# Kernel optimization log

Measured on AMD Instinct MI355X. Metric: run time of the kernel, lower is better.

Reference implementation:

```python
import jax, jax.numpy as jnp
import numpy as np

B, L, N, D = 16, 4096, 1024, 256
EPS = 1e-5
NEG = -1e9


def setup_inputs() -> dict:
    key = jax.random.key(0)
    k1, k2, k3 = jax.random.split(key, 3)
    exp_f = jax.random.normal(k1, (B, L, D), dtype=jnp.float32)
    Q = jax.random.normal(k2, (B, N, D), dtype=jnp.float32)
    attn_mask = jax.random.randint(k3, (B, L, N), 0, 2).astype(jnp.bool_)
    gamma = jnp.ones((D,), dtype=jnp.float32)
    beta = jnp.zeros((D,), dtype=jnp.float32)
    return {"exp_f": exp_f, "Q": Q, "attn_mask": attn_mask, "gamma": gamma, "beta": beta}


def layer_norm(x, gamma, beta):
    mu = jnp.mean(x, axis=-1, keepdims=True)
    var = jnp.mean(jnp.square(x - mu), axis=-1, keepdims=True)
    return (x - mu) * jax.lax.rsqrt(var + EPS) * gamma + beta


def reference(exp_f, Q, attn_mask, gamma, beta):
    d_k = Q.shape[-1]
    scale = 1.0 / np.sqrt(d_k).astype(np.float32)
    # scores: [B, L, N] = exp_f @ Q^T / sqrt(d)
    scores = jnp.einsum('bld,bnd->bln', exp_f, Q) * scale
    scores = jnp.where(attn_mask, jnp.float32(NEG), scores)
    # transpose to [B, N, L], softmax over L (text positions)
    attn = jax.nn.softmax(scores.transpose(0, 2, 1), axis=-1)
    # context: [B, N, D]
    context = jnp.einsum('bnl,bld->bnd', attn, exp_f)
    return layer_norm(Q + context, gamma, beta)
```

## Files before the change

kernel.cpp:

```cpp
#include <hip/hip_runtime.h>
#include <hip/hip_bf16.h>
#include <math.h>

typedef short bf16x8 __attribute__((ext_vector_type(8)));
typedef float f32x4 __attribute__((ext_vector_type(4)));
typedef unsigned int u32;
typedef unsigned short u16;

#define B_ 16
#define L_ 4096
#define N_ 1024
#define D_ 256
#define EPS_ 1e-5f
#define NEG_ -1.0e9f
#define LOG2E_ 1.4426950408889634f
#define THR_ 8.0f

#define LBLK 32
#define ESTR2 264
#define TSTR2 40
#define PSTR2 40

__device__ __forceinline__ u32 pk2(float x, float y) {
  __hip_bfloat16 hx = __float2bfloat16(x), hy = __float2bfloat16(y);
  return (u32)reinterpret_cast<unsigned short&>(hx) |
         ((u32)reinterpret_cast<unsigned short&>(hy) << 16);
}
__device__ __forceinline__ float bf2f(u16 u) {
  return __uint_as_float(((u32)u) << 16);
}

__global__ __launch_bounds__(256)
void prep_kernel(const float* __restrict__ ef, __hip_bfloat16* __restrict__ et,
                 __hip_bfloat16* __restrict__ ebf, int write_ebf) {
  __shared__ float T[64][65];
  const int tid = threadIdx.x;
  const int bid = blockIdx.x;
  const int b  = bid >> 8;
  const int lt = (bid >> 2) & 63;
  const int dt = bid & 3;
  {
    const int r = tid & 63, s = tid >> 6;
    const float* src = ef + ((size_t)b * L_ + lt * 64 + r) * D_ + dt * 64 + s * 16;
    float v[16];
    #pragma unroll
    for (int k = 0; k < 4; ++k) {
      float4 f = *reinterpret_cast<const float4*>(src + 4 * k);
      v[4*k] = f.x; v[4*k+1] = f.y; v[4*k+2] = f.z; v[4*k+3] = f.w;
    }
    #pragma unroll
    for (int m = 0; m < 16; ++m) T[r][s * 16 + m] = v[m];
    if (write_ebf) {
      u32 w[8];
      #pragma unroll
      for (int p = 0; p < 8; ++p) w[p] = pk2(v[2*p], v[2*p+1]);
      __hip_bfloat16* dst = ebf + ((size_t)b * L_ + lt * 64 + r) * D_ + dt * 64 + s * 16;
      *reinterpret_cast<uint4*>(dst)     = *reinterpret_cast<uint4*>(&w[0]);
      *reinterpret_cast<uint4*>(dst + 8) = *reinterpret_cast<uint4*>(&w[4]);
    }
  }
  __syncthreads();
  {
    const int dcol = tid & 63, s2 = tid >> 6;
    float v[16];
    #pragma unroll
    for (int m = 0; m < 16; ++m) v[m] = T[s2 * 16 + m][dcol];
    u32 w[8];
    #pragma unroll
    for (int p = 0; p < 8; ++p) w[p] = pk2(v[2*p], v[2*p+1]);
    __hip_bfloat16* dst = et + ((size_t)b * D_ + dt * 64 + dcol) * L_ + lt * 64 + s2 * 16;
    *reinterpret_cast<uint4*>(dst)     = *reinterpret_cast<uint4*>(&w[0]);
    *reinterpret_cast<uint4*>(dst + 8) = *reinterpret_cast<uint4*>(&w[4]);
  }
}

__global__ __launch_bounds__(256, 2)
void attn_part2(const float* __restrict__ ef, const float* __restrict__ q,
                const int* __restrict__ msk, const __hip_bfloat16* __restrict__ et,
                const __hip_bfloat16* __restrict__ ebf, int use_ebf, int slog,
                __hip_bfloat16* __restrict__ opart,
                float* __restrict__ mpart, float* __restrict__ lpart) {
  extern __shared__ char smem[];
  __hip_bfloat16* EL  = (__hip_bfloat16*)smem;
  __hip_bfloat16* TL  = EL + LBLK * ESTR2;
  __hip_bfloat16* PLb = TL + 256 * TSTR2;

  const int tid  = threadIdx.x;
  const int wid  = tid >> 6;
  const int lane = tid & 63;
  const int g    = lane >> 4;
  const int c    = lane & 15;

  const int S   = 1 << slog;
  const int nb  = 128 << slog;
  const int raw = blockIdx.x;
  const int cpx = nb >> 3;
  const int bs  = (raw & 7) * cpx + (raw >> 3);
  const int nt   = bs & 7;
  const int rest = bs >> 3;
  const int s    = rest & (S - 1);
  const int b    = rest >> slog;

  const int lsplit = L_ >> slog;
  const int lbase  = s * lsplit;
  const int n0w    = nt * 128 + wid * 32;

  bf16x8 qf[2][8];
  #pragma unroll
  for (int h = 0; h < 2; ++h) {
    const float* qrow = q + ((size_t)b * N_ + n0w + 16*h + c) * D_;
    #pragma unroll
    for (int dk = 0; dk < 8; ++dk) {
      float4 a  = *reinterpret_cast<const float4*>(qrow + 32 * dk + 8 * g);
      float4 b2 = *reinterpret_cast<const float4*>(qrow + 32 * dk + 8 * g + 4);
      u32 w[4] = {pk2(a.x, a.y), pk2(a.z, a.w), pk2(b2.x, b2.y), pk2(b2.z, b2.w)};
      qf[h][dk] = *reinterpret_cast<bf16x8*>(w);
    }
  }

  f32x4 oacc[2][16];
  float m_run[2], l_run[2];
  #pragma unroll
  for (int h = 0; h < 2; ++h) {
    m_run[h] = -INFINITY; l_run[h] = 0.f;
    #pragma unroll
    for (int j = 0; j < 16; ++j) oacc[h][j] = (f32x4){0.f, 0.f, 0.f, 0.f};
  }

  __hip_bfloat16* PLw = PLb + wid * (2 * 16 * PSTR2);
  const float scale = 0.0625f;
  const int ntiles = lsplit / LBLK;

  for (int t = 0; t < ntiles; ++t) {
    const int l0 = lbase + t * LBLK;

    __syncthreads();

    #pragma unroll
    for (int p = 0; p < 4; ++p) {
      const int unit = tid + 256 * p;
      const int row = unit >> 5, iu = unit & 31;
      if (use_ebf) {
        *reinterpret_cast<uint4*>(EL + row * ESTR2 + iu * 8) =
            *reinterpret_cast<const uint4*>(ebf + ((size_t)b * L_ + l0 + row) * D_ + iu * 8);
      } else {
        const float* src = ef + ((size_t)b * L_ + l0 + row) * D_ + iu * 8;
        float4 a  = *reinterpret_cast<const float4*>(src);
        float4 b2 = *reinterpret_cast<const float4*>(src + 4);
        u32 w[4] = {pk2(a.x, a.y), pk2(a.z, a.w), pk2(b2.x, b2.y), pk2(b2.z, b2.w)};
        *reinterpret_cast<uint4*>(EL + row * ESTR2 + iu * 8) =
            *reinterpret_cast<uint4*>(w);
      }
    }
    #pragma unroll
    for (int p = 0; p < 4; ++p) {
      const int unit = tid + 256 * p;
      const int dr = unit >> 2, iu = unit & 3;
      *reinterpret_cast<uint4*>(TL + dr * TSTR2 + iu * 8) =
          *reinterpret_cast<const uint4*>(et + ((size_t)b * D_ + dr) * L_ + l0 + iu * 8);
    }

    int mv[16];
    #pragma unroll
    for (int h = 0; h < 2; ++h)
      #pragma unroll
      for (int tt = 0; tt < 2; ++tt)
        #pragma unroll
        for (int r = 0; r < 4; ++r)
          mv[8*h + 4*tt + r] =
              msk[((size_t)b * L_ + l0 + 16*tt + 4*g + r) * N_ + n0w + 16*h + c];

    __syncthreads();

    float sv[2][8];
    #pragma unroll
    for (int tt = 0; tt < 2; ++tt) {
      f32x4 s0 = (f32x4){0.f, 0.f, 0.f, 0.f};
      f32x4 s1 = (f32x4){0.f, 0.f, 0.f, 0.f};
      #pragma unroll
      for (int dk = 0; dk < 8; ++dk) {
        bf16x8 af = *reinterpret_cast<const bf16x8*>(EL + (16*tt + c) * ESTR2 + 32*dk + 8*g);
        s0 = __builtin_amdgcn_mfma_f32_16x16x32_bf16(af, qf[0][dk], s0, 0, 0, 0);
        s1 = __builtin_amdgcn_mfma_f32_16x16x32_bf16(af, qf[1][dk], s1, 0, 0, 0);
      }
      #pragma unroll
      for (int r = 0; r < 4; ++r) {
        float v0 = s0[r] * scale;
        float v1 = s1[r] * scale;
        if (mv[4*tt + r])     v0 = NEG_;
        if (mv[8 + 4*tt + r]) v1 = NEG_;
        sv[0][4*tt + r] = v0;
        sv[1][4*tt + r] = v1;
      }
    }

    #pragma unroll
    for (int h = 0; h < 2; ++h) {
      float tm = sv[h][0];
      #pragma unroll
      for (int i = 1; i < 8; ++i) tm = fmaxf(tm, sv[h][i]);
      tm = fmaxf(tm, __shfl_xor(tm, 16));
      tm = fmaxf(tm, __shfl_xor(tm, 32));
      if (!__all(tm - m_run[h] <= THR_)) {
        const float mn = fmaxf(m_run[h], tm);
        const float alpha = __builtin_amdgcn_exp2f((m_run[h] - mn) * LOG2E_);
        l_run[h] *= alpha;
        float ar[4];
        #pragma unroll
        for (int r = 0; r < 4; ++r) ar[r] = __shfl(alpha, 4*g + r, 64);
        #pragma unroll
        for (int j = 0; j < 16; ++j)
          #pragma unroll
          for (int r = 0; r < 4; ++r) oacc[h][j][r] *= ar[r];
        m_run[h] = mn;
      }
      float ts = 0.f;
      #pragma unroll
      for (int i = 0; i < 8; ++i) {
        sv[h][i] = __builtin_amdgcn_exp2f((sv[h][i] - m_run[h]) * LOG2E_);
        ts += sv[h][i];
      }
      ts += __shfl_xor(ts, 16);
      ts += __shfl_xor(ts, 32);
      l_run[h] += ts;
      #pragma unroll
      for (int tt = 0; tt < 2; ++tt) {
        uint2 w;
        w.x = pk2(sv[h][4*tt+0], sv[h][4*tt+1]);
        w.y = pk2(sv[h][4*tt+2], sv[h][4*tt+3]);
        *reinterpret_cast<uint2*>(PLw + h * 16 * PSTR2 + c * PSTR2 + 16*tt + 4*g) = w;
      }
    }

    bf16x8 pa0 = *reinterpret_cast<const bf16x8*>(PLw + c * PSTR2 + 8*g);
    bf16x8 pa1 = *reinterpret_cast<const bf16x8*>(PLw + 16 * PSTR2 + c * PSTR2 + 8*g);
    #pragma unroll
    for (int j = 0; j < 16; ++j) {
      bf16x8 bfr = *reinterpret_cast<const bf16x8*>(TL + (16*j + c) * TSTR2 + 8*g);
      oacc[0][j] = __builtin_amdgcn_mfma_f32_16x16x32_bf16(pa0, bfr, oacc[0][j], 0, 0, 0);
      oacc[1][j] = __builtin_amdgcn_mfma_f32_16x16x32_bf16(pa1, bfr, oacc[1][j], 0, 0, 0);
    }
  }

  const size_t slot = (size_t)rest * 8 + nt;
  __hip_bfloat16* ob = opart + slot * (128 * 256);
  #pragma unroll
  for (int h = 0; h < 2; ++h) {
    float invl[4];
    #pragma unroll
    for (int r = 0; r < 4; ++r) invl[r] = 1.f / __shfl(l_run[h], 4*g + r, 64);
    #pragma unroll
    for (int r = 0; r < 4; ++r) {
      const int row = wid * 32 + 16*h + 4*g + r;
      #pragma unroll
      for (int j = 0; j < 16; ++j)
        ob[(size_t)row * 256 + 16*j + c] = __float2bfloat16(oacc[h][j][r] * invl[r]);
    }
  }
  if (g == 0) {
    #pragma unroll
    for (int h = 0; h < 2; ++h) {
      mpart[slot * 128 + wid * 32 + 16*h + c] = m_run[h];
      lpart[slot * 128 + wid * 32 + 16*h + c] = l_run[h];
    }
  }
}

__global__ __launch_bounds__(256)
void combine_ln2(const float* __restrict__ q, const float* __restrict__ gamma,
                 const float* __restrict__ beta,
                 const __hip_bfloat16* __restrict__ opart,
                 const float* __restrict__ mpart, const float* __restrict__ lpart,
                 int S, float* __restrict__ out) {
  const int tid = threadIdx.x, wid = tid >> 6, lane = tid & 63;
  const int row = blockIdx.x * 4 + wid;
  const int b = row >> 10, n = row & 1023;
  const int ntile = n >> 7, nl = n & 127;

  float M = -INFINITY;
  for (int s = 0; s < S; ++s) {
    const size_t slot = (size_t)(b * S + s) * 8 + ntile;
    M = fmaxf(M, mpart[slot * 128 + nl]);
  }
  float W = 0.f;
  float4 o = make_float4(0.f, 0.f, 0.f, 0.f);
  for (int s = 0; s < S; ++s) {
    const size_t slot = (size_t)(b * S + s) * 8 + ntile;
    const float w = __builtin_amdgcn_exp2f((mpart[slot * 128 + nl] - M) * LOG2E_) *
                    lpart[slot * 128 + nl];
    W += w;
    ushort4 ov = *reinterpret_cast<const ushort4*>(
        opart + (slot * 128 + nl) * 256 + lane * 4);
    o.x += w * bf2f(ov.x); o.y += w * bf2f(ov.y);
    o.z += w * bf2f(ov.z); o.w += w * bf2f(ov.w);
  }
  const float invW = 1.f / W;
  float4 qv = *reinterpret_cast<const float4*>(q + ((size_t)b * N_ + n) * D_ + lane * 4);
  float4 x;
  x.x = qv.x + o.x * invW; x.y = qv.y + o.y * invW;
  x.z = qv.z + o.z * invW; x.w = qv.w + o.w * invW;

  float sum = x.x + x.y + x.z + x.w;
  sum += __shfl_xor(sum, 1);  sum += __shfl_xor(sum, 2);
  sum += __shfl_xor(sum, 4);  sum += __shfl_xor(sum, 8);
  sum += __shfl_xor(sum, 16); sum += __shfl_xor(sum, 32);
  const float mu = sum * (1.f / 256.f);
  float dx, v2 = 0.f;
  dx = x.x - mu; v2 += dx * dx; dx = x.y - mu; v2 += dx * dx;
  dx = x.z - mu; v2 += dx * dx; dx = x.w - mu; v2 += dx * dx;
  v2 += __shfl_xor(v2, 1);  v2 += __shfl_xor(v2, 2);
  v2 += __shfl_xor(v2, 4);  v2 += __shfl_xor(v2, 8);
  v2 += __shfl_xor(v2, 16); v2 += __shfl_xor(v2, 32);
  const float rs = rsqrtf(v2 * (1.f / 256.f) + EPS_);
  float4 gv = *reinterpret_cast<const float4*>(gamma + lane * 4);
  float4 bv = *reinterpret_cast<const float4*>(beta + lane * 4);
  float4 y;
  y.x = (x.x - mu) * rs * gv.x + bv.x;
  y.y = (x.y - mu) * rs * gv.y + bv.y;
  y.z = (x.z - mu) * rs * gv.z + bv.z;
  y.w = (x.w - mu) * rs * gv.w + bv.w;
  *reinterpret_cast<float4*>(out + ((size_t)b * N_ + n) * D_ + lane * 4) = y;
}

#define QSTRIDE (D_ + 4)
#define PSTRIDF (64 + 4)
__global__ __launch_bounds__(256)
void tgq_fallback(const float* __restrict__ ef, const float* __restrict__ q,
                  const int* __restrict__ msk, const float* __restrict__ gamma,
                  const float* __restrict__ beta, float* __restrict__ out) {
  extern __shared__ float fsm[];
  float* QL = fsm;
  float* EL = QL + 64 * QSTRIDE;
  float* PL = EL + 64 * QSTRIDE;
  const int tid = threadIdx.x, tx = tid & 15, ty = tid >> 4;
  const int b = blockIdx.x >> 4, n0 = (blockIdx.x & 15) * 64;
  {
    const float* qsrc = q + ((size_t)b * N_ + n0) * D_;
    for (int idx = tid; idx < 64 * 64; idx += 256) {
      int row = idx >> 6, c4 = idx & 63;
      *reinterpret_cast<float4*>(&QL[row * QSTRIDE + c4 * 4]) =
          *reinterpret_cast<const float4*>(qsrc + (size_t)row * D_ + c4 * 4);
    }
  }
  float4 O4[4][4]; float m_run[4], l_run[4];
  #pragma unroll
  for (int i = 0; i < 4; ++i) {
    m_run[i] = -INFINITY; l_run[i] = 0.f;
    #pragma unroll
    for (int k = 0; k < 4; ++k) O4[i][k] = make_float4(0.f, 0.f, 0.f, 0.f);
  }
  const float* efb = ef + (size_t)b * L_ * D_;
  const int* mb = msk + (size_t)b * L_ * N_;
  for (int t = 0; t < L_ / 64; ++t) {
    const int l0 = t * 64;
    __syncthreads();
    for (int idx = tid; idx < 64 * 64; idx += 256) {
      int row = idx >> 6, c4 = idx & 63;
      *reinterpret_cast<float4*>(&EL[row * QSTRIDE + c4 * 4]) =
          *reinterpret_cast<const float4*>(efb + (size_t)(l0 + row) * D_ + c4 * 4);
    }
    int4 mvv[4];
    #pragma unroll
    for (int j = 0; j < 4; ++j)
      mvv[j] = *reinterpret_cast<const int4*>(mb + (size_t)(l0 + tx + 16*j) * N_ + n0 + 4*ty);
    __syncthreads();
    float s0[4][4];
    #pragma unroll
    for (int i = 0; i < 4; ++i)
      #pragma unroll
      for (int j = 0; j < 4; ++j) s0[i][j] = 0.f;
    #pragma unroll 4
    for (int dq = 0; dq < 64; ++dq) {
      float4 qv[4], ev[4];
      #pragma unroll
      for (int i = 0; i < 4; ++i)
        qv[i] = *reinterpret_cast<const float4*>(&QL[(4*ty+i) * QSTRIDE + dq*4]);
      #pragma unroll
      for (int j = 0; j < 4; ++j)
        ev[j] = *reinterpret_cast<const float4*>(&EL[(tx+16*j) * QSTRIDE + dq*4]);
      #pragma unroll
      for (int i = 0; i < 4; ++i)
        #pragma unroll
        for (int j = 0; j < 4; ++j)
          s0[i][j] += qv[i].x*ev[j].x + qv[i].y*ev[j].y + qv[i].z*ev[j].z + qv[i].w*ev[j].w;
    }
    #pragma unroll
    for (int i = 0; i < 4; ++i)
      #pragma unroll
      for (int j = 0; j < 4; ++j) {
        float v = s0[i][j] * 0.0625f;
        int mi = (i==0)?mvv[j].x:(i==1)?mvv[j].y:(i==2)?mvv[j].z:mvv[j].w;
        if (mi) v = NEG_;
        s0[i][j] = v;
      }
    #pragma unroll
    for (int i = 0; i < 4; ++i) {
      float mt = fmaxf(fmaxf(s0[i][0], s0[i][1]), fmaxf(s0[i][2], s0[i][3]));
      mt = fmaxf(mt, __shfl_xor(mt,1)); mt = fmaxf(mt, __shfl_xor(mt,2));
      mt = fmaxf(mt, __shfl_xor(mt,4)); mt = fmaxf(mt, __shfl_xor(mt,8));
      float mn = fmaxf(m_run[i], mt);
      float alpha = __builtin_amdgcn_exp2f((m_run[i] - mn) * LOG2E_);
      float tsum = 0.f;
      #pragma unroll
      for (int j = 0; j < 4; ++j) {
        float p = __builtin_amdgcn_exp2f((s0[i][j] - mn) * LOG2E_);
        s0[i][j] = p; tsum += p;
      }
      tsum += __shfl_xor(tsum,1); tsum += __shfl_xor(tsum,2);
      tsum += __shfl_xor(tsum,4); tsum += __shfl_xor(tsum,8);
      l_run[i] = l_run[i] * alpha + tsum; m_run[i] = mn;
      #pragma unroll
      for (int k = 0; k < 4; ++k) {
        O4[i][k].x *= alpha; O4[i][k].y *= alpha; O4[i][k].z *= alpha; O4[i][k].w *= alpha;
      }
    }
    #pragma unroll
    for (int i = 0; i < 4; ++i)
      #pragma unroll
      for (int j = 0; j < 4; ++j)
        PL[(4*ty+i) * PSTRIDF + tx + 16*j] = s0[i][j];
    __syncthreads();
    #pragma unroll 2
    for (int l4 = 0; l4 < 16; ++l4) {
      float4 p4[4];
      #pragma unroll
      for (int i = 0; i < 4; ++i)
        p4[i] = *reinterpret_cast<const float4*>(&PL[(4*ty+i) * PSTRIDF + 4*l4]);
      #pragma unroll
      for (int cc = 0; cc < 4; ++cc) {
        float4 e4[4];
        #pragma unroll
        for (int k = 0; k < 4; ++k)
          e4[k] = *reinterpret_cast<const float4*>(&EL[(4*l4+cc) * QSTRIDE + 4*tx + 64*k]);
        #pragma unroll
        for (int i = 0; i < 4; ++i) {
          float pc = (cc==0)?p4[i].x:(cc==1)?p4[i].y:(cc==2)?p4[i].z:p4[i].w;
          #pragma unroll
          for (int k = 0; k < 4; ++k) {
            O4[i][k].x += pc*e4[k].x; O4[i][k].y += pc*e4[k].y;
            O4[i][k].z += pc*e4[k].z; O4[i][k].w += pc*e4[k].w;
          }
        }
      }
    }
  }
  float* outb = out + ((size_t)b * N_ + n0) * D_;
  #pragma unroll
  for (int i = 0; i < 4; ++i) {
    const int row = 4*ty + i;
    const float inv_l = 1.f / l_run[i];
    float4 xv[4]; float sum = 0.f;
    #pragma unroll
    for (int k = 0; k < 4; ++k) {
      const int d = 4*tx + 64*k;
      float4 qv = *reinterpret_cast<const float4*>(&QL[row * QSTRIDE + d]);
      xv[k].x = qv.x + O4[i][k].x*inv_l; xv[k].y = qv.y + O4[i][k].y*inv_l;
      xv[k].z = qv.z + O4[i][k].z*inv_l; xv[k].w = qv.w + O4[i][k].w*inv_l;
      sum += xv[k].x + xv[k].y + xv[k].z + xv[k].w;
    }
    sum += __shfl_xor(sum,1); sum += __shfl_xor(sum,2);
    sum += __shfl_xor(sum,4); sum += __shfl_xor(sum,8);
    const float mu = sum * (1.f / 256.f);
    float s2 = 0.f;
    #pragma unroll
    for (int k = 0; k < 4; ++k) {
      float dxx;
      dxx = xv[k].x-mu; s2 += dxx*dxx; dxx = xv[k].y-mu; s2 += dxx*dxx;
      dxx = xv[k].z-mu; s2 += dxx*dxx; dxx = xv[k].w-mu; s2 += dxx*dxx;
    }
    s2 += __shfl_xor(s2,1); s2 += __shfl_xor(s2,2);
    s2 += __shfl_xor(s2,4); s2 += __shfl_xor(s2,8);
    const float rs = rsqrtf(s2 * (1.f / 256.f) + EPS_);
    #pragma unroll
    for (int k = 0; k < 4; ++k) {
      const int d = 4*tx + 64*k;
      float4 gg = *reinterpret_cast<const float4*>(gamma + d);
      float4 be = *reinterpret_cast<const float4*>(beta + d);
      float4 y;
      y.x = (xv[k].x-mu)*rs*gg.x + be.x; y.y = (xv[k].y-mu)*rs*gg.y + be.y;
      y.z = (xv[k].z-mu)*rs*gg.z + be.z; y.w = (xv[k].w-mu)*rs*gg.w + be.w;
      *reinterpret_cast<float4*>(outb + (size_t)row * D_ + d) = y;
    }
  }
}

extern "C" void kernel_launch(void* const* d_in, const int* in_sizes, int n_in,
                              void* d_out, int out_size, void* d_ws, size_t ws_size,
                              hipStream_t stream) {
  const float* ef    = (const float*)d_in[0];
  const float* q     = (const float*)d_in[1];
  const int*   m     = (const int*)d_in[2];
  const float* gamma = (const float*)d_in[3];
  const float* beta  = (const float*)d_in[4];
  float* out         = (float*)d_out;

  const size_t et_b  = (size_t)B_ * D_ * L_ * 2;
  const size_t ebf_b = (size_t)B_ * L_ * D_ * 2;
  auto part_bytes = [](int S) {
    const size_t slots = (size_t)B_ * S * 8;
    return slots * 128 * 256 * 2 + 2 * slots * 128 * 4;
  };

  int slog = -1, use_ebf = 0;
  if      (ws_size >= et_b + ebf_b + part_bytes(8)) { slog = 3; use_ebf = 1; }
  else if (ws_size >= et_b + part_bytes(8))         { slog = 3; use_ebf = 0; }
  else if (ws_size >= et_b + ebf_b + part_bytes(4)) { slog = 2; use_ebf = 1; }
  else if (ws_size >= et_b + part_bytes(4))         { slog = 2; use_ebf = 0; }

  if (slog < 0) {
    const size_t lds = (size_t)(64*QSTRIDE + 64*QSTRIDE + 64*PSTRIDF) * sizeof(float);
    (void)hipFuncSetAttribute(reinterpret_cast<const void*>(tgq_fallback),
                              hipFuncAttributeMaxDynamicSharedMemorySize, (int)lds);
    tgq_fallback<<<dim3(256), dim3(256), lds, stream>>>(ef, q, m, gamma, beta, out);
    return;
  }

  const int S = 1 << slog;
  __hip_bfloat16* et  = (__hip_bfloat16*)d_ws;
  __hip_bfloat16* ebf = use_ebf ? (et + (size_t)B_ * D_ * L_) : nullptr;
  const size_t slots = (size_t)B_ * S * 8;
  __hip_bfloat16* opart = (__hip_bfloat16*)((char*)d_ws + et_b + (use_ebf ? ebf_b : 0));
  float* mpart = (float*)(opart + slots * 128 * 256);
  float* lpart = mpart + slots * 128;

  prep_kernel<<<dim3(4096), dim3(256), 0, stream>>>(ef, et, ebf, use_ebf);

  const size_t lds1 =
      (size_t)(LBLK * ESTR2 + 256 * TSTR2 + 4 * 2 * 16 * PSTR2) * 2;
  attn_part2<<<dim3(128 * S), dim3(256), lds1, stream>>>(
      ef, q, m, et, ebf, use_ebf, slog, opart, mpart, lpart);

  combine_ln2<<<dim3(4096), dim3(256), 0, stream>>>(
      q, gamma, beta, opart, mpart, lpart, S, out);
}
```

Before: 315.3 us.

## Double-buffer attention tiles via direct global-to-LDS loads with swizzled layout

Adds a new attention kernel that stages the bf16 exp_f tile and the transposed tile straight into LDS with global_load_lds, double-buffered so the next tile's load overlaps the current tile's MFMA work. The prep kernel now writes the bf16 copy with an XOR swizzle per row, so the unpadded LDS layout avoids bank conflicts on the MFMA operand reads. It also removes one barrier per tile and raises wave priority around the MFMA sections. The costs are more LDS per block (two buffers each) and dropping the two-blocks-per-CU launch bound, which may reduce occupancy.

```diff
diff --git a/kernel.cpp b/kernel.cpp
--- a/kernel.cpp
+++ b/kernel.cpp
@@ -17,9 +17,9 @@
 #define THR_ 8.0f
 
 #define LBLK 32
+#define PSTR2 40
 #define ESTR2 264
 #define TSTR2 40
-#define PSTR2 40
 
 __device__ __forceinline__ u32 pk2(float x, float y) {
   __hip_bfloat16 hx = __float2bfloat16(x), hy = __float2bfloat16(y);
@@ -54,9 +54,11 @@
       u32 w[8];
       #pragma unroll
       for (int p = 0; p < 8; ++p) w[p] = pk2(v[2*p], v[2*p+1]);
-      __hip_bfloat16* dst = ebf + ((size_t)b * L_ + lt * 64 + r) * D_ + dt * 64 + s * 16;
-      *reinterpret_cast<uint4*>(dst)     = *reinterpret_cast<uint4*>(&w[0]);
-      *reinterpret_cast<uint4*>(dst + 8) = *reinterpret_cast<uint4*>(&w[4]);
+      __hip_bfloat16* dstrow = ebf + ((size_t)b * L_ + lt * 64 + r) * D_;
+      const int u0 = dt * 8 + s * 2;
+      const int sw = r & 7;
+      *reinterpret_cast<uint4*>(dstrow + (size_t)(u0 ^ sw) * 8)       = *reinterpret_cast<uint4*>(&w[0]);
+      *reinterpret_cast<uint4*>(dstrow + (size_t)((u0 + 1) ^ sw) * 8) = *reinterpret_cast<uint4*>(&w[4]);
     }
   }
   __syncthreads();
@@ -74,16 +76,16 @@
   }
 }
 
-__global__ __launch_bounds__(256, 2)
-void attn_part2(const float* __restrict__ ef, const float* __restrict__ q,
-                const int* __restrict__ msk, const __hip_bfloat16* __restrict__ et,
-                const __hip_bfloat16* __restrict__ ebf, int use_ebf, int slog,
+__global__ __launch_bounds__(256)
+void attn_part3(const float* __restrict__ q, const int* __restrict__ msk,
+                const __hip_bfloat16* __restrict__ et,
+                const __hip_bfloat16* __restrict__ ebf, int slog,
                 __hip_bfloat16* __restrict__ opart,
                 float* __restrict__ mpart, float* __restrict__ lpart) {
   extern __shared__ char smem[];
-  __hip_bfloat16* EL  = (__hip_bfloat16*)smem;
-  __hip_bfloat16* TL  = EL + LBLK * ESTR2;
-  __hip_bfloat16* PLb = TL + 256 * TSTR2;
+  __hip_bfloat16* ELb = (__hip_bfloat16*)smem;
+  __hip_bfloat16* TLb = ELb + 2 * 32 * 256;
+  __hip_bfloat16* PLb = TLb + 2 * 256 * 32;
 
   const int tid  = threadIdx.x;
   const int wid  = tid >> 6;
@@ -104,6 +106,7 @@
   const int lsplit = L_ >> slog;
   const int lbase  = s * lsplit;
   const int n0w    = nt * 128 + wid * 32;
+  const int ntiles = lsplit / LBLK;
 
   bf16x8 qf[2][8];
   #pragma unroll
@@ -129,36 +132,45 @@
 
   __hip_bfloat16* PLw = PLb + wid * (2 * 16 * PSTR2);
   const float scale = 0.0625f;
-  const int ntiles = lsplit / LBLK;
+
+  auto STAGE = [&](int tindex, int bufi) {
+    const int l0 = lbase + tindex * LBLK;
+    __hip_bfloat16* ELd = ELb + bufi * (32 * 256);
+    __hip_bfloat16* TLd = TLb + bufi * (256 * 32);
+    #pragma unroll
+    for (int p = 0; p < 4; ++p) {
+      const int u   = (wid * 4 + p) * 64 + lane;
+      const int row = u >> 5, iu = u & 31;
+      const __hip_bfloat16* src =
+          ebf + ((size_t)b * L_ + l0 + row) * D_ + (size_t)iu * 8;
+      __builtin_amdgcn_global_load_lds(
+          (const __attribute__((address_space(1))) void*)src,
+          (__attribute__((address_space(3))) void*)(ELd + (size_t)(wid * 4 + p) * 512),
+          16, 0, 0);
+    }
+    #pragma unroll
+    for (int p = 0; p < 4; ++p) {
+      const int u  = (wid * 4 + p) * 64 + lane;
+      const int dr = u >> 2, iu = u & 3;
+      const __hip_bfloat16* src =
+          et + ((size_t)b * D_ + dr) * L_ + l0 + iu * 8;
+      __builtin_amdgcn_global_load_lds(
+          (const __attribute__((address_space(1))) void*)src,
+          (__attribute__((address_space(3))) void*)(TLd + (size_t)(wid * 4 + p) * 512),
+          16, 0, 0);
+    }
+  };
+
+  STAGE(0, 0);
+  int cur = 0;
 
   for (int t = 0; t < ntiles; ++t) {
+    __syncthreads();
+    if (t + 1 < ntiles) STAGE(t + 1, cur ^ 1);
+
     const int l0 = lbase + t * LBLK;
-
-    __syncthreads();
-
-    #pragma unroll
-    for (int p = 0; p < 4; ++p) {
-      const int unit = tid + 256 * p;
-      const int row = unit >> 5, iu = unit & 31;
-      if (use_ebf) {
-        *reinterpret_cast<uint4*>(EL + row * ESTR2 + iu * 8) =
-            *reinterpret_cast<const uint4*>(ebf + ((size_t)b * L_ + l0 + row) * D_ + iu * 8);
-      } else {
-        const float* src = ef + ((size_t)b * L_ + l0 + row) * D_ + iu * 8;
-        float4 a  = *reinterpret_cast<const float4*>(src);
-        float4 b2 = *reinterpret_cast<const float4*>(src + 4);
-        u32 w[4] = {pk2(a.x, a.y), pk2(a.z, a.w), pk2(b2.x, b2.y), pk2(b2.z, b2.w)};
-        *reinterpret_cast<uint4*>(EL + row * ESTR2 + iu * 8) =
-            *reinterpret_cast<uint4*>(w);
-      }
-    }
-    #pragma unroll
-    for (int p = 0; p < 4; ++p) {
-      const int unit = tid + 256 * p;
-      const int dr = unit >> 2, iu = unit & 3;
-      *reinterpret_cast<uint4*>(TL + dr * TSTR2 + iu * 8) =
-          *reinterpret_cast<const uint4*>(et + ((size_t)b * D_ + dr) * L_ + l0 + iu * 8);
-    }
+    const __hip_bfloat16* ELc = ELb + cur * (32 * 256);
+    const __hip_bfloat16* TLc = TLb + cur * (256 * 32);
 
     int mv[16];
     #pragma unroll
@@ -170,16 +182,17 @@
           mv[8*h + 4*tt + r] =
               msk[((size_t)b * L_ + l0 + 16*tt + 4*g + r) * N_ + n0w + 16*h + c];
 
-    __syncthreads();
-
     float sv[2][8];
+    __builtin_amdgcn_s_setprio(1);
     #pragma unroll
     for (int tt = 0; tt < 2; ++tt) {
       f32x4 s0 = (f32x4){0.f, 0.f, 0.f, 0.f};
       f32x4 s1 = (f32x4){0.f, 0.f, 0.f, 0.f};
+      const __hip_bfloat16* Erow = ELc + (16*tt + c) * 256;
+      const int sw = c & 7;
       #pragma unroll
       for (int dk = 0; dk < 8; ++dk) {
-        bf16x8 af = *reinterpret_cast<const bf16x8*>(EL + (16*tt + c) * ESTR2 + 32*dk + 8*g);
+        bf16x8 af = *reinterpret_cast<const bf16x8*>(Erow + (size_t)((4*dk + g) ^ sw) * 8);
         s0 = __builtin_amdgcn_mfma_f32_16x16x32_bf16(af, qf[0][dk], s0, 0, 0, 0);
         s1 = __builtin_amdgcn_mfma_f32_16x16x32_bf16(af, qf[1][dk], s1, 0, 0, 0);
       }
@@ -193,6 +206,7 @@
         sv[1][4*tt + r] = v1;
       }
     }
+    __builtin_amdgcn_s_setprio(0);
 
     #pragma unroll
     for (int h = 0; h < 2; ++h) {
@@ -234,6 +248,181 @@
 
     bf16x8 pa0 = *reinterpret_cast<const bf16x8*>(PLw + c * PSTR2 + 8*g);
     bf16x8 pa1 = *reinterpret_cast<const bf16x8*>(PLw + 16 * PSTR2 + c * PSTR2 + 8*g);
+    __builtin_amdgcn_s_setprio(1);
+    #pragma unroll
+    for (int j = 0; j < 16; ++j) {
+      bf16x8 bfr = *reinterpret_cast<const bf16x8*>(TLc + (16*j + c) * 32 + 8*g);
+      oacc[0][j] = __builtin_amdgcn_mfma_f32_16x16x32_bf16(pa0, bfr, oacc[0][j], 0, 0, 0);
+      oacc[1][j] = __builtin_amdgcn_mfma_f32_16x16x32_bf16(pa1, bfr, oacc[1][j], 0, 0, 0);
+    }
+    __builtin_amdgcn_s_setprio(0);
+
+    cur ^= 1;
+  }
+
+  const size_t slot = (size_t)rest * 8 + nt;
+  __hip_bfloat16* ob = opart + slot * (128 * 256);
+  #pragma unroll
+  for (int h = 0; h < 2; ++h) {
+    float invl[4];
+    #pragma unroll
+    for (int r = 0; r < 4; ++r) invl[r] = 1.f / __shfl(l_run[h], 4*g + r, 64);
+    #pragma unroll
+    for (int r = 0; r < 4; ++r) {
+      const int row = wid * 32 + 16*h + 4*g + r;
+      #pragma unroll
+      for (int j = 0; j < 16; ++j)
+        ob[(size_t)row * 256 + 16*j + c] = __float2bfloat16(oacc[h][j][r] * invl[r]);
+    }
+  }
+  if (g == 0) {
+    #pragma unroll
+    for (int h = 0; h < 2; ++h) {
+      mpart[slot * 128 + wid * 32 + 16*h + c] = m_run[h];
+      lpart[slot * 128 + wid * 32 + 16*h + c] = l_run[h];
+    }
+  }
+}
+
+__global__ __launch_bounds__(256, 2)
+void attn_part2(const float* __restrict__ ef, const float* __restrict__ q,
+                const int* __restrict__ msk, const __hip_bfloat16* __restrict__ et,
+                int slog, __hip_bfloat16* __restrict__ opart,
+                float* __restrict__ mpart, float* __restrict__ lpart) {
+  extern __shared__ char smem[];
+  __hip_bfloat16* EL  = (__hip_bfloat16*)smem;
+  __hip_bfloat16* TL  = EL + LBLK * ESTR2;
+  __hip_bfloat16* PLb = TL + 256 * TSTR2;
+  const int tid  = threadIdx.x;
+  const int wid  = tid >> 6;
+  const int lane = tid & 63;
+  const int g    = lane >> 4;
+  const int c    = lane & 15;
+  const int S   = 1 << slog;
+  const int nb  = 128 << slog;
+  const int raw = blockIdx.x;
+  const int cpx = nb >> 3;
+  const int bs  = (raw & 7) * cpx + (raw >> 3);
+  const int nt   = bs & 7;
+  const int rest = bs >> 3;
+  const int s    = rest & (S - 1);
+  const int b    = rest >> slog;
+  const int lsplit = L_ >> slog;
+  const int lbase  = s * lsplit;
+  const int n0w    = nt * 128 + wid * 32;
+  bf16x8 qf[2][8];
+  #pragma unroll
+  for (int h = 0; h < 2; ++h) {
+    const float* qrow = q + ((size_t)b * N_ + n0w + 16*h + c) * D_;
+    #pragma unroll
+    for (int dk = 0; dk < 8; ++dk) {
+      float4 a  = *reinterpret_cast<const float4*>(qrow + 32 * dk + 8 * g);
+      float4 b2 = *reinterpret_cast<const float4*>(qrow + 32 * dk + 8 * g + 4);
+      u32 w[4] = {pk2(a.x, a.y), pk2(a.z, a.w), pk2(b2.x, b2.y), pk2(b2.z, b2.w)};
+      qf[h][dk] = *reinterpret_cast<bf16x8*>(w);
+    }
+  }
+  f32x4 oacc[2][16];
+  float m_run[2], l_run[2];
+  #pragma unroll
+  for (int h = 0; h < 2; ++h) {
+    m_run[h] = -INFINITY; l_run[h] = 0.f;
+    #pragma unroll
+    for (int j = 0; j < 16; ++j) oacc[h][j] = (f32x4){0.f, 0.f, 0.f, 0.f};
+  }
+  __hip_bfloat16* PLw = PLb + wid * (2 * 16 * PSTR2);
+  const float scale = 0.0625f;
+  const int ntiles = lsplit / LBLK;
+  for (int t = 0; t < ntiles; ++t) {
+    const int l0 = lbase + t * LBLK;
+    __syncthreads();
+    #pragma unroll
+    for (int p = 0; p < 4; ++p) {
+      const int unit = tid + 256 * p;
+      const int row = unit >> 5, iu = unit & 31;
+      const float* src = ef + ((size_t)b * L_ + l0 + row) * D_ + iu * 8;
+      float4 a  = *reinterpret_cast<const float4*>(src);
+      float4 b2 = *reinterpret_cast<const float4*>(src + 4);
+      u32 w[4] = {pk2(a.x, a.y), pk2(a.z, a.w), pk2(b2.x, b2.y), pk2(b2.z, b2.w)};
+      *reinterpret_cast<uint4*>(EL + row * ESTR2 + iu * 8) = *reinterpret_cast<uint4*>(w);
+    }
+    #pragma unroll
+    for (int p = 0; p < 4; ++p) {
+      const int unit = tid + 256 * p;
+      const int dr = unit >> 2, iu = unit & 3;
+      *reinterpret_cast<uint4*>(TL + dr * TSTR2 + iu * 8) =
+          *reinterpret_cast<const uint4*>(et + ((size_t)b * D_ + dr) * L_ + l0 + iu * 8);
+    }
+    int mv[16];
+    #pragma unroll
+    for (int h = 0; h < 2; ++h)
+      #pragma unroll
+      for (int tt = 0; tt < 2; ++tt)
+        #pragma unroll
+        for (int r = 0; r < 4; ++r)
+          mv[8*h + 4*tt + r] =
+              msk[((size_t)b * L_ + l0 + 16*tt + 4*g + r) * N_ + n0w + 16*h + c];
+    __syncthreads();
+    float sv[2][8];
+    #pragma unroll
+    for (int tt = 0; tt < 2; ++tt) {
+      f32x4 s0 = (f32x4){0.f, 0.f, 0.f, 0.f};
+      f32x4 s1 = (f32x4){0.f, 0.f, 0.f, 0.f};
+      #pragma unroll
+      for (int dk = 0; dk < 8; ++dk) {
+        bf16x8 af = *reinterpret_cast<const bf16x8*>(EL + (16*tt + c) * ESTR2 + 32*dk + 8*g);
+        s0 = __builtin_amdgcn_mfma_f32_16x16x32_bf16(af, qf[0][dk], s0, 0, 0, 0);
+        s1 = __builtin_amdgcn_mfma_f32_16x16x32_bf16(af, qf[1][dk], s1, 0, 0, 0);
+      }
+      #pragma unroll
+      for (int r = 0; r < 4; ++r) {
+        float v0 = s0[r] * scale;
+        float v1 = s1[r] * scale;
+        if (mv[4*tt + r])     v0 = NEG_;
+        if (mv[8 + 4*tt + r]) v1 = NEG_;
+        sv[0][4*tt + r] = v0;
+        sv[1][4*tt + r] = v1;
+      }
+    }
+    #pragma unroll
+    for (int h = 0; h < 2; ++h) {
+      float tm = sv[h][0];
+      #pragma unroll
+      for (int i = 1; i < 8; ++i) tm = fmaxf(tm, sv[h][i]);
+      tm = fmaxf(tm, __shfl_xor(tm, 16));
+      tm = fmaxf(tm, __shfl_xor(tm, 32));
+      if (!__all(tm - m_run[h] <= THR_)) {
+        const float mn = fmaxf(m_run[h], tm);
+        const float alpha = __builtin_amdgcn_exp2f((m_run[h] - mn) * LOG2E_);
+        l_run[h] *= alpha;
+        float ar[4];
+        #pragma unroll
+        for (int r = 0; r < 4; ++r) ar[r] = __shfl(alpha, 4*g + r, 64);
+        #pragma unroll
+        for (int j = 0; j < 16; ++j)
+          #pragma unroll
+          for (int r = 0; r < 4; ++r) oacc[h][j][r] *= ar[r];
+        m_run[h] = mn;
+      }
+      float ts = 0.f;
+      #pragma unroll
+      for (int i = 0; i < 8; ++i) {
+        sv[h][i] = __builtin_amdgcn_exp2f((sv[h][i] - m_run[h]) * LOG2E_);
+        ts += sv[h][i];
+      }
+      ts += __shfl_xor(ts, 16);
+      ts += __shfl_xor(ts, 32);
+      l_run[h] += ts;
+      #pragma unroll
+      for (int tt = 0; tt < 2; ++tt) {
+        uint2 w;
+        w.x = pk2(sv[h][4*tt+0], sv[h][4*tt+1]);
+        w.y = pk2(sv[h][4*tt+2], sv[h][4*tt+3]);
+        *reinterpret_cast<uint2*>(PLw + h * 16 * PSTR2 + c * PSTR2 + 16*tt + 4*g) = w;
+      }
+    }
+    bf16x8 pa0 = *reinterpret_cast<const bf16x8*>(PLw + c * PSTR2 + 8*g);
+    bf16x8 pa1 = *reinterpret_cast<const bf16x8*>(PLw + 16 * PSTR2 + c * PSTR2 + 8*g);
     #pragma unroll
     for (int j = 0; j < 16; ++j) {
       bf16x8 bfr = *reinterpret_cast<const bf16x8*>(TL + (16*j + c) * TSTR2 + 8*g);
@@ -241,7 +430,6 @@
       oacc[1][j] = __builtin_amdgcn_mfma_f32_16x16x32_bf16(pa1, bfr, oacc[1][j], 0, 0, 0);
     }
   }
-
   const size_t slot = (size_t)rest * 8 + nt;
   __hip_bfloat16* ob = opart + slot * (128 * 256);
   #pragma unroll
@@ -501,11 +689,11 @@
     return slots * 128 * 256 * 2 + 2 * slots * 128 * 4;
   };
 
-  int slog = -1, use_ebf = 0;
-  if      (ws_size >= et_b + ebf_b + part_bytes(8)) { slog = 3; use_ebf = 1; }
-  else if (ws_size >= et_b + part_bytes(8))         { slog = 3; use_ebf = 0; }
-  else if (ws_size >= et_b + ebf_b + part_bytes(4)) { slog = 2; use_ebf = 1; }
-  else if (ws_size >= et_b + part_bytes(4))         { slog = 2; use_ebf = 0; }
+  int slog = -1, use_gll = 0;
+  if      (ws_size >= et_b + ebf_b + part_bytes(8)) { slog = 3; use_gll = 1; }
+  else if (ws_size >= et_b + ebf_b + part_bytes(4)) { slog = 2; use_gll = 1; }
+  else if (ws_size >= et_b + part_bytes(8))         { slog = 3; use_gll = 0; }
+  else if (ws_size >= et_b + part_bytes(4))         { slog = 2; use_gll = 0; }
 
   if (slog < 0) {
     const size_t lds = (size_t)(64*QSTRIDE + 64*QSTRIDE + 64*PSTRIDF) * sizeof(float);
@@ -517,18 +705,26 @@
 
   const int S = 1 << slog;
   __hip_bfloat16* et  = (__hip_bfloat16*)d_ws;
-  __hip_bfloat16* ebf = use_ebf ? (et + (size_t)B_ * D_ * L_) : nullptr;
+  __hip_bfloat16* ebf = use_gll ? (et + (size_t)B_ * D_ * L_) : nullptr;
   const size_t slots = (size_t)B_ * S * 8;
-  __hip_bfloat16* opart = (__hip_bfloat16*)((char*)d_ws + et_b + (use_ebf ? ebf_b : 0));
+  __hip_bfloat16* opart =
+      (__hip_bfloat16*)((char*)d_ws + et_b + (use_gll ? ebf_b : 0));
   float* mpart = (float*)(opart + slots * 128 * 256);
   float* lpart = mpart + slots * 128;
 
-  prep_kernel<<<dim3(4096), dim3(256), 0, stream>>>(ef, et, ebf, use_ebf);
-
-  const size_t lds1 =
-      (size_t)(LBLK * ESTR2 + 256 * TSTR2 + 4 * 2 * 16 * PSTR2) * 2;
-  attn_part2<<<dim3(128 * S), dim3(256), lds1, stream>>>(
-      ef, q, m, et, ebf, use_ebf, slog, opart, mpart, lpart);
+  prep_kernel<<<dim3(4096), dim3(256), 0, stream>>>(ef, et, ebf, use_gll);
+
+  if (use_gll) {
+    const size_t lds1 = (size_t)(2 * 32 * 256 + 2 * 256 * 32 + 4 * 2 * 16 * PSTR2) * 2;
+    (void)hipFuncSetAttribute(reinterpret_cast<const void*>(attn_part3),
+                              hipFuncAttributeMaxDynamicSharedMemorySize, (int)lds1);
+    attn_part3<<<dim3(128 * S), dim3(256), lds1, stream>>>(
+        q, m, et, ebf, slog, opart, mpart, lpart);
+  } else {
+    const size_t lds1 = (size_t)(LBLK * ESTR2 + 256 * TSTR2 + 4 * 2 * 16 * PSTR2) * 2;
+    attn_part2<<<dim3(128 * S), dim3(256), lds1, stream>>>(
+        ef, q, m, et, slog, opart, mpart, lpart);
+  }
 
   combine_ln2<<<dim3(4096), dim3(256), 0, stream>>>(
       q, gamma, beta, opart, mpart, lpart, S, out);
```

Result: faster. 296.5 us (-6.0%).
